# Optimization experiments

Measured on AMD Instinct MI355X. Metric: run time of the kernel, lower is better.

## Reference

```python
import jax, jax.numpy as jnp
import numpy as np

ATTRACTION_W = 1.0
REPULSION_W = 1.0
BETA_POS_W = 1.0
BETA_NEG_W = 0.5
K_INST = 256  # max number of distinct instance ids (slice ids)


def setup_inputs() -> dict:
    key = jax.random.key(0)
    B, N, D, K = 4, 65536, 256, K_INST
    k1, k2, k3 = jax.random.split(key, 3)
    beta = jax.random.normal(k1, (B, N, 1), jnp.float32)
    embed = jax.random.normal(k2, (B, N, D), jnp.float32)
    sid = jax.random.randint(k3, (B, N), -1, K)  # -1 = background
    # force exactly one condensation point per instance: hit i (<K) -> sid=i, is_cp
    sid = sid.at[:, :K].set(jnp.broadcast_to(jnp.arange(K), (B, K)))
    is_cp = jnp.zeros((B, N), bool).at[:, :K].set(True)
    return {"beta": beta, "embed": embed, "slice_id": sid, "is_cp": is_cp}


def _loss_single(beta, emb, sid, cp):
    # beta: (N,) logits, emb: (N,D), sid: (N,) int, cp: (N,) bool
    N = sid.shape[0]
    valid = sid >= 0
    cpv = cp & valid  # condensation points with a valid instance id
    # BCE-with-logits: target 1 -> softplus(-x), target 0 -> softplus(x)
    pos = jnp.sum(jnp.where(cpv, jax.nn.softplus(-beta), 0.0)) / jnp.maximum(cpv.sum(), 1)
    noncp = ~cp
    neg = jnp.sum(jnp.where(noncp, jax.nn.softplus(beta), 0.0)) / jnp.maximum(noncp.sum(), 1)
    beta_loss = BETA_POS_W * pos + BETA_NEG_W * neg

    # first CP hit index per instance (segment-min over CP hits), N = "no CP"
    sid_c = jnp.where(valid, sid, 0)
    idx = jnp.arange(N)
    first_cp = jnp.full((K_INST,), N, jnp.int32).at[sid_c].min(
        jnp.where(cpv, idx, N).astype(jnp.int32))
    has_cp = first_cp < N
    cp_emb = emb[jnp.minimum(first_cp, N - 1)]  # (K, D), garbage where no CP

    # attraction: sum over instances of mean ||emb - inst_cp||^2
    d2 = jnp.sum((emb - cp_emb[sid_c]) ** 2, axis=-1)  # (N,)
    w = valid & has_cp[sid_c]
    seg_sum = jnp.zeros((K_INST,), jnp.float32).at[sid_c].add(jnp.where(w, d2, 0.0))
    seg_cnt = jnp.zeros((K_INST,), jnp.float32).at[sid_c].add(w.astype(jnp.float32))
    attraction = jnp.sum(jnp.where(seg_cnt > 0, seg_sum / jnp.maximum(seg_cnt, 1.0), 0.0))
    attraction = attraction * ATTRACTION_W

    # repulsion: mean exp(-||cp_i - cp_j||^2) over all CP pairs (incl. diagonal)
    pd2 = jnp.sum((cp_emb[:, None, :] - cp_emb[None, :, :]) ** 2, axis=-1)  # (K,K)
    pmask = has_cp[:, None] & has_cp[None, :]
    M = has_cp.sum()
    rep = jnp.sum(jnp.where(pmask, jnp.exp(-pd2), 0.0)) / jnp.maximum(M * M, 1)
    rep = jnp.where(M > 1, rep * REPULSION_W, 0.0)

    loss = beta_loss + attraction + rep
    ok = (valid.sum() > 0) & (cpv.sum() > 0)
    return jnp.where(ok, loss, 0.0), ok


def reference(beta, embed, slice_id, is_cp):
    losses, oks = jax.vmap(_loss_single)(beta.squeeze(-1), embed, slice_id, is_cp)
    cnt = oks.sum()
    return jnp.where(cnt > 0, losses.sum() / jnp.maximum(cnt, 1), 0.0)
```

## Files before the change

### kernel.cpp

```cpp
#include <hip/hip_runtime.h>
#include <math.h>

#define K_INST 256
#define ATTRACTION_W 1.0f
#define REPULSION_W 1.0f
#define BETA_POS_W 1.0f
#define BETA_NEG_W 0.5f

typedef float f32x4 __attribute__((ext_vector_type(4)));

__device__ inline float softplusf(float x) {
    return fmaxf(x, 0.f) + log1pf(expf(-fabsf(x)));
}

__device__ inline float waveReduceSumF(float v) {
    for (int o = 32; o; o >>= 1) v += __shfl_xor(v, o);
    return v;
}
__device__ inline int waveReduceSumI(int v) {
    for (int o = 32; o; o >>= 1) v += __shfl_xor(v, o);
    return v;
}

__global__ void init_kernel(int* first_cp, float* seg_sum, int* seg_cnt,
                            float* pos_sum, float* neg_sum, float* rep_sum,
                            int* cpv_cnt, int* noncp_cnt, int* valid_cnt,
                            int N, int B) {
    int idx = blockIdx.x * blockDim.x + threadIdx.x;
    if (idx < B * K_INST) {
        first_cp[idx] = N;
        seg_sum[idx] = 0.f;
        seg_cnt[idx] = 0;
    }
    if (idx < B) {
        pos_sum[idx] = 0.f; neg_sum[idx] = 0.f; rep_sum[idx] = 0.f;
        cpv_cnt[idx] = 0; noncp_cnt[idx] = 0; valid_cnt[idx] = 0;
    }
}

__global__ void stats_kernel(const float* __restrict__ beta,
                             const int* __restrict__ sid,
                             const int* __restrict__ is_cp,
                             int* first_cp,
                             float* pos_sum, float* neg_sum,
                             int* cpv_cnt, int* noncp_cnt, int* valid_cnt,
                             int N) {
    int b = blockIdx.y;
    int i = blockIdx.x * blockDim.x + threadIdx.x;
    size_t gi = (size_t)b * N + i;
    int s = sid[gi];
    int cp = is_cp[gi];
    float x = beta[gi];

    bool valid = s >= 0;
    bool cpv = cp && valid;
    float pos = 0.f, neg = 0.f;
    int c_cpv = 0, c_non = 0, c_val = valid ? 1 : 0;
    if (cpv) {
        pos = softplusf(-x);
        c_cpv = 1;
        atomicMin(&first_cp[b * K_INST + s], i);
    }
    if (!cp) {
        neg = softplusf(x);
        c_non = 1;
    }

    __shared__ float sf[2][4];
    __shared__ int si[3][4];
    pos = waveReduceSumF(pos);
    neg = waveReduceSumF(neg);
    c_cpv = waveReduceSumI(c_cpv);
    c_non = waveReduceSumI(c_non);
    c_val = waveReduceSumI(c_val);
    int wave = threadIdx.x >> 6, lane = threadIdx.x & 63;
    if (lane == 0) {
        sf[0][wave] = pos; sf[1][wave] = neg;
        si[0][wave] = c_cpv; si[1][wave] = c_non; si[2][wave] = c_val;
    }
    __syncthreads();
    if (threadIdx.x == 0) {
        float p = sf[0][0] + sf[0][1] + sf[0][2] + sf[0][3];
        float n = sf[1][0] + sf[1][1] + sf[1][2] + sf[1][3];
        int a = si[0][0] + si[0][1] + si[0][2] + si[0][3];
        int c = si[1][0] + si[1][1] + si[1][2] + si[1][3];
        int v = si[2][0] + si[2][1] + si[2][2] + si[2][3];
        if (p != 0.f) atomicAdd(&pos_sum[b], p);
        if (n != 0.f) atomicAdd(&neg_sum[b], n);
        if (a) atomicAdd(&cpv_cnt[b], a);
        if (c) atomicAdd(&noncp_cnt[b], c);
        if (v) atomicAdd(&valid_cnt[b], v);
    }
}

__global__ void gather_kernel(const float* __restrict__ embed,
                              const int* __restrict__ first_cp,
                              float* __restrict__ cp_emb,
                              float* __restrict__ cp_embT, int N) {
    int b = blockIdx.y;
    int k = blockIdx.x;
    int src = first_cp[b * K_INST + k];
    if (src >= N) src = N - 1;
    int lane = threadIdx.x;
    const float* embB = embed + (size_t)b * N * 256;
    f32x4 v = ((const f32x4*)(embB + (size_t)src * 256))[lane];
    ((f32x4*)(cp_emb + ((size_t)b * K_INST + k) * 256))[lane] = v;
    float* T = cp_embT + (size_t)b * K_INST * 256;
    int d = lane * 4;
    T[(size_t)(d + 0) * 256 + k] = v[0];
    T[(size_t)(d + 1) * 256 + k] = v[1];
    T[(size_t)(d + 2) * 256 + k] = v[2];
    T[(size_t)(d + 3) * 256 + k] = v[3];
}

__device__ inline float sel8f(const float* v, int lane) {
    float a0 = (lane & 1) ? v[1] : v[0];
    float a1 = (lane & 1) ? v[3] : v[2];
    float a2 = (lane & 1) ? v[5] : v[4];
    float a3 = (lane & 1) ? v[7] : v[6];
    float b0 = (lane & 2) ? a1 : a0;
    float b1 = (lane & 2) ? a3 : a2;
    return (lane & 4) ? b1 : b0;
}
__device__ inline int sel8i(const int* v, int lane) {
    int a0 = (lane & 1) ? v[1] : v[0];
    int a1 = (lane & 1) ? v[3] : v[2];
    int a2 = (lane & 1) ? v[5] : v[4];
    int a3 = (lane & 1) ? v[7] : v[6];
    int b0 = (lane & 2) ? a1 : a0;
    int b1 = (lane & 2) ? a3 : a2;
    return (lane & 4) ? b1 : b0;
}

__global__ void attraction_repulsion_kernel(
        const float* __restrict__ embed,
        const int* __restrict__ sid,
        const int* __restrict__ first_cp,
        const float* __restrict__ cp_emb,
        const float* __restrict__ cp_embT,
        float* seg_sum, int* seg_cnt, float* rep_sum,
        int N, int atr_blocks) {
    int b = blockIdx.y;
    __shared__ __align__(16) char smem[8448];
    __shared__ float sf[4];

    const float* cpB = cp_emb + (size_t)b * K_INST * 256;
    const int* fcB = first_cp + b * K_INST;

    if (blockIdx.x < 32) {
        float (*srow)[264] = (float(*)[264])smem;
        int i0 = blockIdx.x * 8;
        const float* T = cp_embT + (size_t)b * K_INST * 256;
        {
            int r = threadIdx.x >> 5, cc = (threadIdx.x & 31) * 8;
            f32x4 a = *(const f32x4*)(cpB + (size_t)(i0 + r) * 256 + cc);
            f32x4 bv = *(const f32x4*)(cpB + (size_t)(i0 + r) * 256 + cc + 4);
            srow[r][cc + 0] = a[0]; srow[r][cc + 1] = a[1];
            srow[r][cc + 2] = a[2]; srow[r][cc + 3] = a[3];
            srow[r][cc + 4] = bv[0]; srow[r][cc + 5] = bv[1];
            srow[r][cc + 6] = bv[2]; srow[r][cc + 7] = bv[3];
        }
        __syncthreads();

        int j = threadIdx.x;
        bool has_j = fcB[j] < N;
        float acc[8] = {0.f, 0.f, 0.f, 0.f, 0.f, 0.f, 0.f, 0.f};
        for (int d = 0; d < 256; d += 2) {
            float v0 = T[(size_t)d * 256 + j];
            float v1 = T[(size_t)(d + 1) * 256 + j];
            #pragma unroll
            for (int r = 0; r < 8; ++r) {
                float f0 = srow[r][d] - v0;
                float f1 = srow[r][d + 1] - v1;
                acc[r] += f0 * f0 + f1 * f1;
            }
        }
        float val = 0.f;
        #pragma unroll
        for (int r = 0; r < 8; ++r) {
            bool has_i = fcB[i0 + r] < N;
            if (has_i && has_j) val += expf(-acc[r]);
        }
        val = waveReduceSumF(val);
        int wave = threadIdx.x >> 6, lane = threadIdx.x & 63;
        if (lane == 0) sf[wave] = val;
        __syncthreads();
        if (threadIdx.x == 0)
            atomicAdd(&rep_sum[b], sf[0] + sf[1] + sf[2] + sf[3]);
    } else {
        float* s_sum = (float*)smem;
        int* s_cnt = (int*)(smem + 1024);
        for (int k = threadIdx.x; k < K_INST; k += blockDim.x) { s_sum[k] = 0.f; s_cnt[k] = 0; }
        __syncthreads();

        int bx = blockIdx.x - 32;
        int wave = threadIdx.x >> 6;
        int lane = threadIdx.x & 63;
        int wid = bx * 4 + wave;
        int stride = atr_blocks * 4 * 8;

        const float* embB = embed + (size_t)b * N * 256;
        const int* sidB = sid + (size_t)b * N;

        int i = wid * 8;
        int4 sa = make_int4(0, 0, 0, 0), sb = make_int4(0, 0, 0, 0);
        if (i < N) {
            sa = *(const int4*)(sidB + i);
            sb = *(const int4*)(sidB + i + 4);
        }
        while (i < N) {
            int ss[8] = {sa.x, sa.y, sa.z, sa.w, sb.x, sb.y, sb.z, sb.w};

            f32x4 e[8];
            #pragma unroll
            for (int j = 0; j < 8; ++j)
                e[j] = *(const f32x4*)(embB + (size_t)(i + j) * 256 + lane * 4);
            f32x4 c[8];
            #pragma unroll
            for (int j = 0; j < 8; ++j) {
                int sc = ss[j] < 0 ? 0 : ss[j];
                c[j] = *(const f32x4*)(cpB + (size_t)sc * 256 + lane * 4);
            }
            int inext = i + stride;
            int4 na = make_int4(0, 0, 0, 0), nb = make_int4(0, 0, 0, 0);
            if (inext < N) {
                na = *(const int4*)(sidB + inext);
                nb = *(const int4*)(sidB + inext + 4);
            }

            float v[8];
            #pragma unroll
            for (int j = 0; j < 8; ++j) {
                float d0 = e[j][0] - c[j][0], d1 = e[j][1] - c[j][1];
                float d2 = e[j][2] - c[j][2], d3 = e[j][3] - c[j][3];
                v[j] = d0 * d0 + d1 * d1 + d2 * d2 + d3 * d3;
            }
            #pragma unroll
            for (int o = 1; o <= 4; o <<= 1) {
                #pragma unroll
                for (int j = 0; j < 8; ++j) v[j] += __shfl_xor(v[j], o);
            }
            float w = sel8f(v, lane & 7);
            #pragma unroll
            for (int o = 8; o <= 32; o <<= 1) w += __shfl_xor(w, o);
            if (lane < 8) {
                int s_sel = sel8i(ss, lane);
                if (s_sel >= 0) {
                    atomicAdd(&s_sum[s_sel], w);
                    atomicAdd(&s_cnt[s_sel], 1);
                }
            }
            sa = na; sb = nb;
            i = inext;
        }
        __syncthreads();
        for (int k = threadIdx.x; k < K_INST; k += blockDim.x) {
            if (s_cnt[k]) {
                atomicAdd(&seg_sum[b * K_INST + k], s_sum[k]);
                atomicAdd(&seg_cnt[b * K_INST + k], s_cnt[k]);
            }
        }
    }
}

__global__ void final_kernel(const int* __restrict__ first_cp,
                             const float* __restrict__ seg_sum,
                             const int* __restrict__ seg_cnt,
                             const float* __restrict__ pos_sum,
                             const float* __restrict__ neg_sum,
                             const float* __restrict__ rep_sum,
                             const int* __restrict__ cpv_cnt,
                             const int* __restrict__ noncp_cnt,
                             const int* __restrict__ valid_cnt,
                             float* out, int N, int B) {
    __shared__ float s_att[4];
    __shared__ int s_m[4];
    float loss_sum = 0.f;
    int ok_cnt = 0;
    int wave = threadIdx.x >> 6, lane = threadIdx.x & 63;
    for (int b = 0; b < B; ++b) {
        int k = threadIdx.x;
        int fc = first_cp[b * K_INST + k];
        int has = (fc < N) ? 1 : 0;
        int cnt = seg_cnt[b * K_INST + k];
        float att = (has && cnt > 0) ? (seg_sum[b * K_INST + k] / (float)cnt) : 0.f;
        att = waveReduceSumF(att);
        has = waveReduceSumI(has);
        if (lane == 0) { s_att[wave] = att; s_m[wave] = has; }
        __syncthreads();
        if (threadIdx.x == 0) {
            float attraction = (s_att[0] + s_att[1] + s_att[2] + s_att[3]) * ATTRACTION_W;
            int M = s_m[0] + s_m[1] + s_m[2] + s_m[3];
            float pos = pos_sum[b] / fmaxf((float)cpv_cnt[b], 1.f);
            float neg = neg_sum[b] / fmaxf((float)noncp_cnt[b], 1.f);
            float beta_loss = BETA_POS_W * pos + BETA_NEG_W * neg;
            float rep = 0.f;
            if (M > 1) {
                float mm = (float)M * (float)M;
                rep = (rep_sum[b] / fmaxf(mm, 1.f)) * REPULSION_W;
            }
            float loss = beta_loss + attraction + rep;
            bool ok = (valid_cnt[b] > 0) && (cpv_cnt[b] > 0);
            if (ok) { loss_sum += loss; ok_cnt += 1; }
        }
        __syncthreads();
    }
    if (threadIdx.x == 0) {
        out[0] = (ok_cnt > 0) ? (loss_sum / (float)ok_cnt) : 0.f;
    }
}

extern "C" void kernel_launch(void* const* d_in, const int* in_sizes, int n_in,
                              void* d_out, int out_size, void* d_ws, size_t ws_size,
                              hipStream_t stream) {
    const float* beta  = (const float*)d_in[0];
    const float* embed = (const float*)d_in[1];
    const int* sid     = (const int*)d_in[2];
    const int* is_cp   = (const int*)d_in[3];
    float* out = (float*)d_out;

    const int N = 65536;
    const int B = in_sizes[0] / N;
    (void)n_in; (void)out_size; (void)ws_size;

    char* ws = (char*)d_ws;
    int*   first_cp  = (int*)(ws + 0);
    float* seg_sum   = (float*)(ws + 4096);
    int*   seg_cnt   = (int*)(ws + 8192);
    float* pos_sum   = (float*)(ws + 12288);
    float* neg_sum   = (float*)(ws + 12352);
    float* rep_sum   = (float*)(ws + 12416);
    int*   cpv_cnt   = (int*)(ws + 12480);
    int*   noncp_cnt = (int*)(ws + 12544);
    int*   valid_cnt = (int*)(ws + 12608);
    float* cp_emb    = (float*)(ws + 16384);
    float* cp_embT   = (float*)(ws + 16384 + (size_t)B * K_INST * 256 * 4);

    init_kernel<<<dim3((B * K_INST + 255) / 256), dim3(256), 0, stream>>>(
        first_cp, seg_sum, seg_cnt, pos_sum, neg_sum, rep_sum,
        cpv_cnt, noncp_cnt, valid_cnt, N, B);

    stats_kernel<<<dim3(N / 256, B), dim3(256), 0, stream>>>(
        beta, sid, is_cp, first_cp, pos_sum, neg_sum,
        cpv_cnt, noncp_cnt, valid_cnt, N);

    gather_kernel<<<dim3(K_INST, B), dim3(64), 0, stream>>>(
        embed, first_cp, cp_emb, cp_embT, N);

    const int atr_blocks = 480;
    attraction_repulsion_kernel<<<dim3(32 + atr_blocks, B), dim3(256), 0, stream>>>(
        embed, sid, first_cp, cp_emb, cp_embT,
        seg_sum, seg_cnt, rep_sum, N, atr_blocks);

    final_kernel<<<dim3(1), dim3(256), 0, stream>>>(
        first_cp, seg_sum, seg_cnt, pos_sum, neg_sum, rep_sum,
        cpv_cnt, noncp_cnt, valid_cnt, out, N, B);
}
```

Measured before the change: 107.9 us.

## Software-pipeline embed loads in attraction loop and shrink grid

Restructures the attraction loop so the next iteration's 8 embedding rows and slice ids are loaded into registers while the current rows are reduced, which is register double buffering. This is meant to hide global memory latency in the embedding stream. Launch bounds of 256 threads with 4 blocks per SM are added, and the attraction grid drops from 480 to 224 blocks per batch so each wave runs more iterations. The extra live registers risk spills or lower occupancy, and the smaller grid may not keep all CUs busy.

```diff
diff --git a/kernel.cpp b/kernel.cpp
--- a/kernel.cpp
+++ b/kernel.cpp
@@ -132,7 +132,7 @@
     return (lane & 4) ? b1 : b0;
 }
 
-__global__ void attraction_repulsion_kernel(
+__global__ void __launch_bounds__(256, 4) attraction_repulsion_kernel(
         const float* __restrict__ embed,
         const int* __restrict__ sid,
         const int* __restrict__ first_cp,
@@ -194,64 +194,73 @@
         __syncthreads();
 
         int bx = blockIdx.x - 32;
-        int wave = threadIdx.x >> 6;
         int lane = threadIdx.x & 63;
-        int wid = bx * 4 + wave;
+        int wid = bx * 4 + (threadIdx.x >> 6);
         int stride = atr_blocks * 4 * 8;
 
         const float* embB = embed + (size_t)b * N * 256;
         const int* sidB = sid + (size_t)b * N;
 
         int i = wid * 8;
-        int4 sa = make_int4(0, 0, 0, 0), sb = make_int4(0, 0, 0, 0);
         if (i < N) {
-            sa = *(const int4*)(sidB + i);
-            sb = *(const int4*)(sidB + i + 4);
-        }
-        while (i < N) {
+            int4 sa = *(const int4*)(sidB + i);
+            int4 sb = *(const int4*)(sidB + i + 4);
             int ss[8] = {sa.x, sa.y, sa.z, sa.w, sb.x, sb.y, sb.z, sb.w};
-
-            f32x4 e[8];
+            f32x4 e[8], c[8];
             #pragma unroll
             for (int j = 0; j < 8; ++j)
                 e[j] = *(const f32x4*)(embB + (size_t)(i + j) * 256 + lane * 4);
-            f32x4 c[8];
             #pragma unroll
             for (int j = 0; j < 8; ++j) {
                 int sc = ss[j] < 0 ? 0 : ss[j];
                 c[j] = *(const f32x4*)(cpB + (size_t)sc * 256 + lane * 4);
             }
             int inext = i + stride;
-            int4 na = make_int4(0, 0, 0, 0), nb = make_int4(0, 0, 0, 0);
-            if (inext < N) {
-                na = *(const int4*)(sidB + inext);
-                nb = *(const int4*)(sidB + inext + 4);
-            }
-
-            float v[8];
-            #pragma unroll
-            for (int j = 0; j < 8; ++j) {
-                float d0 = e[j][0] - c[j][0], d1 = e[j][1] - c[j][1];
-                float d2 = e[j][2] - c[j][2], d3 = e[j][3] - c[j][3];
-                v[j] = d0 * d0 + d1 * d1 + d2 * d2 + d3 * d3;
-            }
-            #pragma unroll
-            for (int o = 1; o <= 4; o <<= 1) {
-                #pragma unroll
-                for (int j = 0; j < 8; ++j) v[j] += __shfl_xor(v[j], o);
-            }
-            float w = sel8f(v, lane & 7);
-            #pragma unroll
-            for (int o = 8; o <= 32; o <<= 1) w += __shfl_xor(w, o);
-            if (lane < 8) {
-                int s_sel = sel8i(ss, lane);
-                if (s_sel >= 0) {
-                    atomicAdd(&s_sum[s_sel], w);
-                    atomicAdd(&s_cnt[s_sel], 1);
-                }
-            }
-            sa = na; sb = nb;
-            i = inext;
+            while (true) {
+                int4 na = make_int4(0, 0, 0, 0), nb = make_int4(0, 0, 0, 0);
+                f32x4 en[8];
+                bool more = inext < N;
+                if (more) {
+                    na = *(const int4*)(sidB + inext);
+                    nb = *(const int4*)(sidB + inext + 4);
+                    #pragma unroll
+                    for (int j = 0; j < 8; ++j)
+                        en[j] = *(const f32x4*)(embB + (size_t)(inext + j) * 256 + lane * 4);
+                }
+                float v[8];
+                #pragma unroll
+                for (int j = 0; j < 8; ++j) {
+                    float d0 = e[j][0] - c[j][0], d1 = e[j][1] - c[j][1];
+                    float d2 = e[j][2] - c[j][2], d3 = e[j][3] - c[j][3];
+                    v[j] = d0 * d0 + d1 * d1 + d2 * d2 + d3 * d3;
+                }
+                #pragma unroll
+                for (int o = 1; o <= 4; o <<= 1) {
+                    #pragma unroll
+                    for (int j = 0; j < 8; ++j) v[j] += __shfl_xor(v[j], o);
+                }
+                float w = sel8f(v, lane & 7);
+                #pragma unroll
+                for (int o = 8; o <= 32; o <<= 1) w += __shfl_xor(w, o);
+                if (lane < 8) {
+                    int s_sel = sel8i(ss, lane);
+                    if (s_sel >= 0) {
+                        atomicAdd(&s_sum[s_sel], w);
+                        atomicAdd(&s_cnt[s_sel], 1);
+                    }
+                }
+                if (!more) break;
+                ss[0] = na.x; ss[1] = na.y; ss[2] = na.z; ss[3] = na.w;
+                ss[4] = nb.x; ss[5] = nb.y; ss[6] = nb.z; ss[7] = nb.w;
+                #pragma unroll
+                for (int j = 0; j < 8; ++j) {
+                    int sc = ss[j] < 0 ? 0 : ss[j];
+                    c[j] = *(const f32x4*)(cpB + (size_t)sc * 256 + lane * 4);
+                }
+                #pragma unroll
+                for (int j = 0; j < 8; ++j) e[j] = en[j];
+                inext += stride;
+            }
         }
         __syncthreads();
         for (int k = threadIdx.x; k < K_INST; k += blockDim.x) {
@@ -347,7 +356,7 @@
     gather_kernel<<<dim3(K_INST, B), dim3(64), 0, stream>>>(
         embed, first_cp, cp_emb, cp_embT, N);
 
-    const int atr_blocks = 480;
+    const int atr_blocks = 224;
     attraction_repulsion_kernel<<<dim3(32 + atr_blocks, B), dim3(256), 0, stream>>>(
         embed, sid, first_cp, cp_emb, cp_embT,
         seg_sum, seg_cnt, rep_sum, N, atr_blocks);
```

Measured after the change: 123.1 us. +14.1%, slower.
